# Performance work log

Hardware: AMD Instinct MI355X
Metric: run time of the kernel (lower is better)

The kernel has to match this reference:

```python
import jax, jax.numpy as jnp
import numpy as np

K = 3  # kernel size, padding=1, stride=1, dilation=1 (torchvision deform_conv2d defaults used)


def _bilinear_sample(img, y, x):
    """Bilinear sample img (B,H,W) at float coords y,x (B,T,H,W) with zero padding
    outside the image, matching torchvision's deform_conv2d bilinear rule
    (each of the four corner taps is zeroed individually when out of range)."""
    B, H, W = img.shape
    y0f = jnp.floor(y)
    x0f = jnp.floor(x)
    ly = y - y0f  # fractional parts
    lx = x - x0f
    hy = 1.0 - ly
    hx = 1.0 - lx
    y0 = y0f.astype(jnp.int32)
    x0 = x0f.astype(jnp.int32)
    y1 = y0 + 1
    x1 = x0 + 1

    img_flat = img.reshape(B, H * W)

    def corner(yi, xi):
        valid = ((yi >= 0) & (yi < H) & (xi >= 0) & (xi < W)).astype(img.dtype)
        yc = jnp.clip(yi, 0, H - 1)
        xc = jnp.clip(xi, 0, W - 1)
        flat = (yc * W + xc).reshape(B, -1)  # (B, T*H*W)
        g = jax.vmap(lambda im, f: im[f])(img_flat, flat).reshape(yi.shape)
        return g * valid

    v00 = corner(y0, x0)
    v01 = corner(y0, x1)
    v10 = corner(y1, x0)
    v11 = corner(y1, x1)
    return hy * hx * v00 + hy * lx * v01 + ly * hx * v10 + ly * lx * v11


def deform_conv2d_1ch(inp, weight, offset):
    # inp: (B,H,W); weight: (1,1,3,3); offset: (B, 2*K*K, H, W)
    B, H, W = inp.shape
    off = offset.reshape(B, K * K, 2, H, W)
    oy = off[:, :, 0]  # (B,9,H,W) y-offsets
    ox = off[:, :, 1]  # (B,9,H,W) x-offsets
    kh, kw = jnp.meshgrid(jnp.arange(K), jnp.arange(K), indexing='ij')
    ky = (kh.reshape(-1) - 1).astype(inp.dtype)  # pad=1 -> tap offsets in {-1,0,1}
    kx = (kw.reshape(-1) - 1).astype(inp.dtype)
    hh = jnp.arange(H, dtype=inp.dtype)
    ww = jnp.arange(W, dtype=inp.dtype)
    y = hh[None, None, :, None] + ky[None, :, None, None] + oy  # (B,9,H,W)
    x = ww[None, None, None, :] + kx[None, :, None, None] + ox
    sampled = _bilinear_sample(inp, y, x)  # (B,9,H,W)
    wk = weight.reshape(K * K)
    return jnp.einsum('k,bkhw->bhw', wk, sampled)


def setup_inputs() -> dict:
    key = jax.random.key(0)
    k1, k2, k3 = jax.random.split(key, 3)
    B, H, W = 8, 512, 512
    inp = jax.random.normal(k1, (B, H, W), dtype=jnp.float32)
    weight = jax.random.uniform(k2, (1, 1, K, K), dtype=jnp.float32)
    offset = jax.random.uniform(k3, (B, 2 * K * K, H, W), dtype=jnp.float32)
    return {"input": inp, "weight": weight, "offset": offset}


def reference(input, weight, offset):
    return deform_conv2d_1ch(input, weight, offset)
```

## Files before the change

kernel.cpp:

```cpp
#include <hip/hip_runtime.h>

constexpr int K  = 3;
constexpr int Hc = 512, Wc = 512, Bc = 8;
constexpr int HWc = Hc * Wc;

__device__ __forceinline__ float bload(__amdgpu_buffer_rsrc_t r, int vo, int so) {
    return __uint_as_float(__builtin_amdgcn_raw_buffer_load_b32(r, vo, so, 0));
}

#define LOADROW(V0, V1, V2, V3, RB)                                  \
    V0 = bload(irsrc, fbB + (RB),      0);                           \
    V1 = bload(irsrc, fbB + (RB) + 4,  0);                           \
    V2 = bload(irsrc, fbB + (RB) + 8,  0);                           \
    V3 = bload(irsrc, fbB + (RB) + 12, 0);                           \
    V0 = c0 ? V0 : 0.f; V2 = c2 ? V2 : 0.f; V3 = c3 ? V3 : 0.f;

#define TAPROW(A0, A1, A2, A3, B0, B1, B2, B3, KB)                   \
    {                                                                \
        float t, bo;                                                 \
        t  = A0 + ox[KB]     * (A1 - A0);                            \
        bo = B0 + ox[KB]     * (B1 - B0);                            \
        acc += wk[KB]     * (t + oy[KB]     * (bo - t));             \
        t  = A1 + ox[KB + 1] * (A2 - A1);                            \
        bo = B1 + ox[KB + 1] * (B2 - B1);                            \
        acc += wk[KB + 1] * (t + oy[KB + 1] * (bo - t));             \
        t  = A2 + ox[KB + 2] * (A3 - A2);                            \
        bo = B2 + ox[KB + 2] * (B3 - B2);                            \
        acc += wk[KB + 2] * (t + oy[KB + 2] * (bo - t));             \
    }

__global__ __launch_bounds__(256, 8) void deform_conv2d_kernel(
    const float* __restrict__ inp,
    const float* __restrict__ wgt,
    const float* __restrict__ off,
    float* __restrict__ out)
{
    const int p  = blockIdx.x * blockDim.x + threadIdx.x;
    const int b  = p >> 18;
    const int hw = p & (HWc - 1);
    const int h  = hw >> 9;
    const int w  = hw & (Wc - 1);

    __amdgpu_buffer_rsrc_t orsrc = __builtin_amdgcn_make_buffer_rsrc(
        (void*)(off + (size_t)b * (2 * K * K) * HWc), (short)0,
        (2 * K * K) * HWc * 4, 0x00020000);
    __amdgpu_buffer_rsrc_t irsrc = __builtin_amdgcn_make_buffer_rsrc(
        (void*)(inp + (size_t)b * HWc), (short)0, HWc * 4, 0x00020000);

    const int hwB = hw * 4;

    float oy[K * K], ox[K * K];
#pragma unroll
    for (int k = 0; k < K * K; ++k) {
        oy[k] = bload(orsrc, hwB, (2 * k)     * HWc * 4);
        ox[k] = bload(orsrc, hwB, (2 * k + 1) * HWc * 4);
    }

    float mn = fminf(oy[0], ox[0]);
    float mx = fmaxf(oy[0], ox[0]);
#pragma unroll
    for (int k = 1; k < K * K; ++k) {
        mn = fminf(mn, fminf(oy[k], ox[k]));
        mx = fmaxf(mx, fmaxf(oy[k], ox[k]));
    }

    float wk[K * K];
#pragma unroll
    for (int k = 0; k < K * K; ++k) wk[k] = wgt[k];

    float acc = 0.f;

    if (__all((mn >= 0.f) & (mx < 1.f))) {
        const int  fbB = ((h - 1) * Wc + (w - 1)) * 4;
        const bool c0 = (w >= 1);
        const bool c2 = (w <= Wc - 2);
        const bool c3 = (w <= Wc - 3);

        float a0, a1, a2, a3, b0, b1, b2, b3;
        LOADROW(a0, a1, a2, a3, 0)
        LOADROW(b0, b1, b2, b3, Wc * 4)
        TAPROW(a0, a1, a2, a3, b0, b1, b2, b3, 0)
        LOADROW(a0, a1, a2, a3, 2 * Wc * 4)
        TAPROW(b0, b1, b2, b3, a0, a1, a2, a3, 3)
        LOADROW(b0, b1, b2, b3, 3 * Wc * 4)
        TAPROW(a0, a1, a2, a3, b0, b1, b2, b3, 6)
    } else {
#pragma unroll
        for (int k = 0; k < K * K; ++k) {
            const int ky = k / K - 1;
            const int kx = k % K - 1;

            const float y = (float)(h + ky) + oy[k];
            const float x = (float)(w + kx) + ox[k];

            const float y0f = floorf(y);
            const float x0f = floorf(x);
            const float ly = y - y0f, lx = x - x0f;
            const int y0 = (int)y0f, x0 = (int)x0f;

            const int fbB = ((y0 << 9) + x0) * 4;
            float v00 = bload(irsrc, fbB,              0);
            float v01 = bload(irsrc, fbB + 4,          0);
            float v10 = bload(irsrc, fbB + Wc * 4,     0);
            float v11 = bload(irsrc, fbB + Wc * 4 + 4, 0);
            const bool vx0 = (unsigned)x0       < (unsigned)Wc;
            const bool vx1 = (unsigned)(x0 + 1) < (unsigned)Wc;
            v00 = vx0 ? v00 : 0.f;   v10 = vx0 ? v10 : 0.f;
            v01 = vx1 ? v01 : 0.f;   v11 = vx1 ? v11 : 0.f;

            const float top = v00 + lx * (v01 - v00);
            const float bot = v10 + lx * (v11 - v10);
            acc += wk[k] * (top + ly * (bot - top));
        }
    }

    out[p] = acc;
}

extern "C" void kernel_launch(void* const* d_in, const int* in_sizes, int n_in,
                              void* d_out, int out_size, void* d_ws, size_t ws_size,
                              hipStream_t stream)
{
    const float* inp = (const float*)d_in[0];
    const float* wgt = (const float*)d_in[1];
    const float* off = (const float*)d_in[2];
    float* out = (float*)d_out;

    const int npix  = Bc * HWc;
    const int block = 256;
    const int grid  = npix / block;

    deform_conv2d_kernel<<<grid, block, 0, stream>>>(inp, wgt, off, out);
}
```

Before: 35.85 us.

## Compute four pixels per thread with shared 4x7 window and vector loads

Each thread now handles four adjacent output pixels. It loads one 4x7 input window per thread with b32/b128/b64 buffer loads, and the offsets and outputs move as 128-bit vectors. The fast-path check is now done per tap instead of once for all nine. The aim is fewer load instructions and reuse of overlapping input taps across neighbouring pixels. In exchange it uses more registers per thread, lowers the occupancy hint, and launches a quarter as many threads.

```diff
diff --git a/kernel.cpp b/kernel.cpp
--- a/kernel.cpp
+++ b/kernel.cpp
@@ -4,42 +4,31 @@
 constexpr int Hc = 512, Wc = 512, Bc = 8;
 constexpr int HWc = Hc * Wc;
 
-__device__ __forceinline__ float bload(__amdgpu_buffer_rsrc_t r, int vo, int so) {
+typedef __attribute__((ext_vector_type(2))) unsigned int u32x2;
+typedef __attribute__((ext_vector_type(4))) unsigned int u32x4;
+
+__device__ __forceinline__ float bl32(__amdgpu_buffer_rsrc_t r, int vo, int so) {
     return __uint_as_float(__builtin_amdgcn_raw_buffer_load_b32(r, vo, so, 0));
 }
+__device__ __forceinline__ u32x2 bl64(__amdgpu_buffer_rsrc_t r, int vo, int so) {
+    return __builtin_amdgcn_raw_buffer_load_b64(r, vo, so, 0);
+}
+__device__ __forceinline__ u32x4 bl128(__amdgpu_buffer_rsrc_t r, int vo, int so) {
+    return __builtin_amdgcn_raw_buffer_load_b128(r, vo, so, 0);
+}
 
-#define LOADROW(V0, V1, V2, V3, RB)                                  \
-    V0 = bload(irsrc, fbB + (RB),      0);                           \
-    V1 = bload(irsrc, fbB + (RB) + 4,  0);                           \
-    V2 = bload(irsrc, fbB + (RB) + 8,  0);                           \
-    V3 = bload(irsrc, fbB + (RB) + 12, 0);                           \
-    V0 = c0 ? V0 : 0.f; V2 = c2 ? V2 : 0.f; V3 = c3 ? V3 : 0.f;
-
-#define TAPROW(A0, A1, A2, A3, B0, B1, B2, B3, KB)                   \
-    {                                                                \
-        float t, bo;                                                 \
-        t  = A0 + ox[KB]     * (A1 - A0);                            \
-        bo = B0 + ox[KB]     * (B1 - B0);                            \
-        acc += wk[KB]     * (t + oy[KB]     * (bo - t));             \
-        t  = A1 + ox[KB + 1] * (A2 - A1);                            \
-        bo = B1 + ox[KB + 1] * (B2 - B1);                            \
-        acc += wk[KB + 1] * (t + oy[KB + 1] * (bo - t));             \
-        t  = A2 + ox[KB + 2] * (A3 - A2);                            \
-        bo = B2 + ox[KB + 2] * (B3 - B2);                            \
-        acc += wk[KB + 2] * (t + oy[KB + 2] * (bo - t));             \
-    }
-
-__global__ __launch_bounds__(256, 8) void deform_conv2d_kernel(
+__global__ __launch_bounds__(256, 6) void deform_conv2d_kernel(
     const float* __restrict__ inp,
     const float* __restrict__ wgt,
     const float* __restrict__ off,
     float* __restrict__ out)
 {
-    const int p  = blockIdx.x * blockDim.x + threadIdx.x;
-    const int b  = p >> 18;
-    const int hw = p & (HWc - 1);
-    const int h  = hw >> 9;
-    const int w  = hw & (Wc - 1);
+    const int idx = blockIdx.x * blockDim.x + threadIdx.x;
+    const int p4  = idx << 2;
+    const int b   = p4 >> 18;
+    const int hw  = p4 & (HWc - 1);
+    const int h   = hw >> 9;
+    const int w   = hw & (Wc - 1);
 
     __amdgpu_buffer_rsrc_t orsrc = __builtin_amdgcn_make_buffer_rsrc(
         (void*)(off + (size_t)b * (2 * K * K) * HWc), (short)0,
@@ -47,74 +36,89 @@
     __amdgpu_buffer_rsrc_t irsrc = __builtin_amdgcn_make_buffer_rsrc(
         (void*)(inp + (size_t)b * HWc), (short)0, HWc * 4, 0x00020000);
 
-    const int hwB = hw * 4;
-
-    float oy[K * K], ox[K * K];
-#pragma unroll
-    for (int k = 0; k < K * K; ++k) {
-        oy[k] = bload(orsrc, hwB, (2 * k)     * HWc * 4);
-        ox[k] = bload(orsrc, hwB, (2 * k + 1) * HWc * 4);
-    }
-
-    float mn = fminf(oy[0], ox[0]);
-    float mx = fmaxf(oy[0], ox[0]);
-#pragma unroll
-    for (int k = 1; k < K * K; ++k) {
-        mn = fminf(mn, fminf(oy[k], ox[k]));
-        mx = fmaxf(mx, fmaxf(oy[k], ox[k]));
-    }
-
     float wk[K * K];
 #pragma unroll
     for (int k = 0; k < K * K; ++k) wk[k] = wgt[k];
 
-    float acc = 0.f;
+    const int  fbB = ((h - 1) * Wc + (w - 1)) * 4;
+    const bool m0 = (w >= 1);
+    const bool m5 = (w + 4 < Wc);
+    const bool m6 = (w + 5 < Wc);
 
-    if (__all((mn >= 0.f) & (mx < 1.f))) {
-        const int  fbB = ((h - 1) * Wc + (w - 1)) * 4;
-        const bool c0 = (w >= 1);
-        const bool c2 = (w <= Wc - 2);
-        const bool c3 = (w <= Wc - 3);
+    float win[4][7];
+#pragma unroll
+    for (int r = 0; r < 4; ++r) {
+        const int rb = fbB + r * Wc * 4;
+        const float e0 = bl32 (irsrc, rb,      0);
+        const u32x4 md = bl128(irsrc, rb + 4,  0);
+        const u32x2 e5 = bl64 (irsrc, rb + 20, 0);
+        win[r][0] = m0 ? e0 : 0.f;
+        win[r][1] = __uint_as_float(md.x);
+        win[r][2] = __uint_as_float(md.y);
+        win[r][3] = __uint_as_float(md.z);
+        win[r][4] = __uint_as_float(md.w);
+        win[r][5] = m5 ? __uint_as_float(e5.x) : 0.f;
+        win[r][6] = m6 ? __uint_as_float(e5.y) : 0.f;
+    }
 
-        float a0, a1, a2, a3, b0, b1, b2, b3;
-        LOADROW(a0, a1, a2, a3, 0)
-        LOADROW(b0, b1, b2, b3, Wc * 4)
-        TAPROW(a0, a1, a2, a3, b0, b1, b2, b3, 0)
-        LOADROW(a0, a1, a2, a3, 2 * Wc * 4)
-        TAPROW(b0, b1, b2, b3, a0, a1, a2, a3, 3)
-        LOADROW(b0, b1, b2, b3, 3 * Wc * 4)
-        TAPROW(a0, a1, a2, a3, b0, b1, b2, b3, 6)
-    } else {
+    const int hwB = hw * 4;
+    float acc[4] = {0.f, 0.f, 0.f, 0.f};
+
 #pragma unroll
-        for (int k = 0; k < K * K; ++k) {
-            const int ky = k / K - 1;
-            const int kx = k % K - 1;
+    for (int k = 0; k < K * K; ++k) {
+        const int ky = k / K - 1;
+        const int kx = k % K - 1;
 
-            const float y = (float)(h + ky) + oy[k];
-            const float x = (float)(w + kx) + ox[k];
+        const u32x4 oyu = bl128(orsrc, hwB, (2 * k)     * HWc * 4);
+        const u32x4 oxu = bl128(orsrc, hwB, (2 * k + 1) * HWc * 4);
+        const float oya[4] = {__uint_as_float(oyu.x), __uint_as_float(oyu.y),
+                              __uint_as_float(oyu.z), __uint_as_float(oyu.w)};
+        const float oxa[4] = {__uint_as_float(oxu.x), __uint_as_float(oxu.y),
+                              __uint_as_float(oxu.z), __uint_as_float(oxu.w)};
 
-            const float y0f = floorf(y);
-            const float x0f = floorf(x);
-            const float ly = y - y0f, lx = x - x0f;
-            const int y0 = (int)y0f, x0 = (int)x0f;
+        const float mn = fminf(fminf(fminf(oya[0], oya[1]), fminf(oya[2], oya[3])),
+                               fminf(fminf(oxa[0], oxa[1]), fminf(oxa[2], oxa[3])));
+        const float mx = fmaxf(fmaxf(fmaxf(oya[0], oya[1]), fmaxf(oya[2], oya[3])),
+                               fmaxf(fmaxf(oxa[0], oxa[1]), fmaxf(oxa[2], oxa[3])));
 
-            const int fbB = ((y0 << 9) + x0) * 4;
-            float v00 = bload(irsrc, fbB,              0);
-            float v01 = bload(irsrc, fbB + 4,          0);
-            float v10 = bload(irsrc, fbB + Wc * 4,     0);
-            float v11 = bload(irsrc, fbB + Wc * 4 + 4, 0);
-            const bool vx0 = (unsigned)x0       < (unsigned)Wc;
-            const bool vx1 = (unsigned)(x0 + 1) < (unsigned)Wc;
-            v00 = vx0 ? v00 : 0.f;   v10 = vx0 ? v10 : 0.f;
-            v01 = vx1 ? v01 : 0.f;   v11 = vx1 ? v11 : 0.f;
+        if (__all((mn >= 0.f) && (mx < 1.f))) {
+            const int r0 = ky + 1;
+#pragma unroll
+            for (int j = 0; j < 4; ++j) {
+                const int c = j + kx + 1;
+                const float t  = win[r0][c]     + oxa[j] * (win[r0][c + 1]     - win[r0][c]);
+                const float bo = win[r0 + 1][c] + oxa[j] * (win[r0 + 1][c + 1] - win[r0 + 1][c]);
+                acc[j] += wk[k] * (t + oya[j] * (bo - t));
+            }
+        } else {
+#pragma unroll
+            for (int j = 0; j < 4; ++j) {
+                const float y = (float)(h + ky)     + oya[j];
+                const float x = (float)(w + j + kx) + oxa[j];
+                const float y0f = floorf(y), x0f = floorf(x);
+                const float ly = y - y0f,  lx = x - x0f;
+                const int y0 = (int)y0f, x0 = (int)x0f;
 
-            const float top = v00 + lx * (v01 - v00);
-            const float bot = v10 + lx * (v11 - v10);
-            acc += wk[k] * (top + ly * (bot - top));
+                const int cb = ((y0 << 9) + x0) * 4;
+                float v00 = bl32(irsrc, cb,              0);
+                float v01 = bl32(irsrc, cb + 4,          0);
+                float v10 = bl32(irsrc, cb + Wc * 4,     0);
+                float v11 = bl32(irsrc, cb + Wc * 4 + 4, 0);
+                const bool vx0 = (unsigned)x0       < (unsigned)Wc;
+                const bool vx1 = (unsigned)(x0 + 1) < (unsigned)Wc;
+                v00 = vx0 ? v00 : 0.f;   v10 = vx0 ? v10 : 0.f;
+                v01 = vx1 ? v01 : 0.f;   v11 = vx1 ? v11 : 0.f;
+
+                const float top = v00 + lx * (v01 - v00);
+                const float bot = v10 + lx * (v11 - v10);
+                acc[j] += wk[k] * (top + ly * (bot - top));
+            }
         }
     }
 
-    out[p] = acc;
+    float4 o;
+    o.x = acc[0]; o.y = acc[1]; o.z = acc[2]; o.w = acc[3];
+    *reinterpret_cast<float4*>(out + p4) = o;
 }
 
 extern "C" void kernel_launch(void* const* d_in, const int* in_sizes, int n_in,
@@ -126,9 +130,9 @@
     const float* off = (const float*)d_in[2];
     float* out = (float*)d_out;
 
-    const int npix  = Bc * HWc;
+    const int nthreads = Bc * HWc / 4;
     const int block = 256;
-    const int grid  = npix / block;
+    const int grid  = nthreads / block;
 
     deform_conv2d_kernel<<<grid, block, 0, stream>>>(inp, wgt, off, out);
 }
```

Measured after the change: 33.48 us, median of 2. 6.6% less time.
